# Kernel tuning notes

Hardware: AMD Instinct MI355X
Metric: run time of the kernel (lower is better)

The kernel has to match this reference:

```python
import jax, jax.numpy as jnp
import numpy as np

L, B, S, D, F, H = 4, 2, 1024, 1024, 4096, 16
EPS = 1e-5


def setup_inputs() -> dict:
    key = jax.random.key(0)
    ks = jax.random.split(key, 15)
    w = lambda k, shape, s=0.02: (jax.random.normal(k, shape, jnp.float32) * s)
    inp = {
        "x": jax.random.normal(ks[0], (B, S, D), jnp.float32),
        # stacked per-layer params (scanned over leading L axis)
        "ln1_w": jnp.ones((L, D), jnp.float32),
        "ln1_b": jnp.zeros((L, D), jnp.float32),
        "Wq": w(ks[1], (L, D, D)),
        "Wk": w(ks[2], (L, D, D)),
        "Wv": w(ks[3], (L, D, D)),
        "Wo": w(ks[4], (L, D, D)),
        "bo": jnp.zeros((L, D), jnp.float32),
        "ln2_w": jnp.ones((L, D), jnp.float32),
        "ln2_b": jnp.zeros((L, D), jnp.float32),
        "W1": w(ks[5], (L, D, F)),
        "b1": jnp.zeros((L, F), jnp.float32),
        "W2": w(ks[6], (L, F, D)),
        "b2": jnp.zeros((L, D), jnp.float32),
    }
    return inp


def _layernorm(y, w, b):
    m = jnp.mean(y, axis=-1, keepdims=True)
    v = jnp.mean(jnp.square(y - m), axis=-1, keepdims=True)
    return (y - m) * jax.lax.rsqrt(v + EPS) * w + b


def _block(x, p):
    ln1w, ln1b, wq, wk, wv, wo, bo, ln2w, ln2b, w1, b1, w2, b2 = p
    b, s, d = x.shape
    dh = d // H
    scale = dh ** -0.5
    # --- attention sub-block (pre-norm, residual) ---
    h = _layernorm(x, ln1w, ln1b)
    q = (h @ wq).reshape(b, s, H, dh).transpose(0, 2, 1, 3)  # bhsd
    k = (h @ wk).reshape(b, s, H, dh).transpose(0, 2, 1, 3)
    v = (h @ wv).reshape(b, s, H, dh).transpose(0, 2, 1, 3)
    attn = jax.nn.softmax(jnp.einsum("bhqd,bhkd->bhqk", q, k) * scale, axis=-1)
    o = jnp.einsum("bhqk,bhkd->bhqd", attn, v).transpose(0, 2, 1, 3).reshape(b, s, d)
    x = x + (o @ wo + bo)
    # --- FFN sub-block (pre-norm, residual) ---
    h = _layernorm(x, ln2w, ln2b)
    x = x + (jax.nn.gelu(h @ w1 + b1, approximate=False) @ w2 + b2)
    return x, None


def reference(x, ln1_w, ln1_b, Wq, Wk, Wv, Wo, bo, ln2_w, ln2_b, W1, b1, W2, b2):
    xs = (ln1_w, ln1_b, Wq, Wk, Wv, Wo, bo, ln2_w, ln2_b, W1, b1, W2, b2)
    out, _ = jax.lax.scan(_block, x, xs)
    return out
```

## Files before the change

kernel.cpp:

```cpp
#include <hip/hip_runtime.h>
#include <hip/hip_bf16.h>

using bf16   = __bf16;
using bf16x2 = __attribute__((ext_vector_type(2))) __bf16;
using bf16x4 = __attribute__((ext_vector_type(4))) __bf16;
using bf16x8 = __attribute__((ext_vector_type(8))) __bf16;
using f32x4  = __attribute__((ext_vector_type(4))) float;

constexpr int LAYERS = 4;
constexpr int BATCH  = 2;
constexpr int SEQ    = 1024;
constexpr int DIM    = 1024;
constexpr int FF     = 4096;
constexpr int HEADS  = 16;
constexpr int TOK    = BATCH * SEQ;
constexpr int QKVN   = 3 * DIM;
constexpr float EPS  = 1e-5f;

__device__ __forceinline__ void gload_lds16(const void* g, void* l) {
    __builtin_amdgcn_global_load_lds(
        (const __attribute__((address_space(1))) void*)g,
        (__attribute__((address_space(3))) void*)l, 16, 0, 0);
}

__global__ __launch_bounds__(256) void ln_kernel(
    const float* __restrict__ x, const float* __restrict__ g,
    const float* __restrict__ bt, bf16* __restrict__ out)
{
    __shared__ float red[8];
    const int row = blockIdx.x, t = threadIdx.x;
    const float4 v = ((const float4*)(x + (size_t)row * DIM))[t];

    float s = v.x + v.y + v.z + v.w;
    #pragma unroll
    for (int o = 32; o; o >>= 1) s += __shfl_down(s, o, 64);
    if ((t & 63) == 0) red[t >> 6] = s;
    __syncthreads();
    const float mean = (red[0] + red[1] + red[2] + red[3]) * (1.0f / DIM);

    const float dx = v.x - mean, dy = v.y - mean, dz = v.z - mean, dw = v.w - mean;
    float q = dx * dx + dy * dy + dz * dz + dw * dw;
    #pragma unroll
    for (int o = 32; o; o >>= 1) q += __shfl_down(q, o, 64);
    if ((t & 63) == 0) red[4 + (t >> 6)] = q;
    __syncthreads();
    const float var = (red[4] + red[5] + red[6] + red[7]) * (1.0f / DIM);
    const float rstd = rsqrtf(var + EPS);

    const float4 gg = ((const float4*)g)[t];
    const float4 bb = ((const float4*)bt)[t];
    bf16x4 o4;
    o4[0] = (bf16)(dx * rstd * gg.x + bb.x);
    o4[1] = (bf16)(dy * rstd * gg.y + bb.y);
    o4[2] = (bf16)(dz * rstd * gg.z + bb.z);
    o4[3] = (bf16)(dw * rstd * gg.w + bb.w);
    *(bf16x4*)(out + (size_t)row * DIM + t * 4) = o4;
}

template<bool DO_LN>
__global__ __launch_bounds__(256) void lncomb_kernel(
    float* __restrict__ x, const bf16* __restrict__ p,
    const float* __restrict__ bias, const float* __restrict__ g,
    const float* __restrict__ bt, bf16* __restrict__ out)
{
    __shared__ float red[8];
    const int row = blockIdx.x, t = threadIdx.x;
    float4 v = ((const float4*)(x + (size_t)row * DIM))[t];
    const float4 bv = ((const float4*)bias)[t];
    float a0 = bv.x, a1 = bv.y, a2 = bv.z, a3 = bv.w;
    #pragma unroll
    for (int ks = 0; ks < 4; ++ks) {
        const bf16x4 pp = *(const bf16x4*)(p + (size_t)(ks * TOK + row) * DIM + t * 4);
        a0 += (float)pp[0]; a1 += (float)pp[1];
        a2 += (float)pp[2]; a3 += (float)pp[3];
    }
    v.x += a0; v.y += a1; v.z += a2; v.w += a3;
    ((float4*)(x + (size_t)row * DIM))[t] = v;
    if (!DO_LN) return;

    float s = v.x + v.y + v.z + v.w;
    #pragma unroll
    for (int o = 32; o; o >>= 1) s += __shfl_down(s, o, 64);
    if ((t & 63) == 0) red[t >> 6] = s;
    __syncthreads();
    const float mean = (red[0] + red[1] + red[2] + red[3]) * (1.0f / DIM);

    const float dx = v.x - mean, dy = v.y - mean, dz = v.z - mean, dw = v.w - mean;
    float q = dx * dx + dy * dy + dz * dz + dw * dw;
    #pragma unroll
    for (int o = 32; o; o >>= 1) q += __shfl_down(q, o, 64);
    if ((t & 63) == 0) red[4 + (t >> 6)] = q;
    __syncthreads();
    const float var = (red[4] + red[5] + red[6] + red[7]) * (1.0f / DIM);
    const float rstd = rsqrtf(var + EPS);

    const float4 gg = ((const float4*)g)[t];
    const float4 bb = ((const float4*)bt)[t];
    bf16x4 o4;
    o4[0] = (bf16)(dx * rstd * gg.x + bb.x);
    o4[1] = (bf16)(dy * rstd * gg.y + bb.y);
    o4[2] = (bf16)(dz * rstd * gg.z + bb.z);
    o4[3] = (bf16)(dw * rstd * gg.w + bb.w);
    *(bf16x4*)(out + (size_t)row * DIM + t * 4) = o4;
}

__global__ __launch_bounds__(256) void wtrans_all_kernel(
    const float* __restrict__ Wq, const float* __restrict__ Wk,
    const float* __restrict__ Wv, const float* __restrict__ Wo,
    const float* __restrict__ W1, const float* __restrict__ W2,
    bf16* __restrict__ wqkvt, bf16* __restrict__ wot,
    bf16* __restrict__ w1t, bf16* __restrict__ w2t)
{
    __shared__ float tile[32][33];
    const int bid = blockIdx.x;
    const float* W; bf16* Wt; int N, K, rowoff, bx, by;
    if (bid < 3072) {
        const int seg = bid >> 10, r = bid & 1023;
        W = (seg == 0) ? Wq : (seg == 1) ? Wk : Wv;
        Wt = wqkvt; N = DIM; K = DIM; rowoff = seg * DIM;
        bx = r & 31; by = r >> 5;
    } else if (bid < 4096) {
        const int r = bid - 3072;
        W = Wo; Wt = wot; N = DIM; K = DIM; rowoff = 0;
        bx = r & 31; by = r >> 5;
    } else if (bid < 8192) {
        const int r = bid - 4096;
        W = W1; Wt = w1t; N = FF; K = DIM; rowoff = 0;
        bx = r & 127; by = r >> 7;
    } else {
        const int r = bid - 8192;
        W = W2; Wt = w2t; N = DIM; K = FF; rowoff = 0;
        bx = r & 31; by = r >> 5;
    }
    const int bn = bx * 32, bk = by * 32;
    const int r = threadIdx.x >> 3, c4 = (threadIdx.x & 7) * 4;
    const float4 v = *(const float4*)(W + (size_t)(bk + r) * N + bn + c4);
    tile[r][c4 + 0] = v.x; tile[r][c4 + 1] = v.y;
    tile[r][c4 + 2] = v.z; tile[r][c4 + 3] = v.w;
    __syncthreads();
    bf16x4 o;
    #pragma unroll
    for (int j = 0; j < 4; ++j) o[j] = (bf16)tile[c4 + j][r];
    *(bf16x4*)(Wt + (size_t)(rowoff + bn + r) * K + bk + c4) = o;
}

template<int EPI, int SK>
__global__ __launch_bounds__(256) void gemm_kernel(
    const bf16* __restrict__ A, const bf16* __restrict__ Bt,
    const float* __restrict__ bias, void* __restrict__ outv,
    int M, int N, int Kfull)
{
    constexpr int MR = 2;
    __shared__ bf16 As[2][128 * 32];
    __shared__ bf16 Bs[2][64 * 32];

    const int t    = threadIdx.x;
    const int lane = t & 63;
    const int w    = t >> 6;
    const int wm   = w * 32;
    const int kg   = lane >> 4, lr = lane & 15;
    const int key  = lr & 3;

    const int nwg = gridDim.x;
    const int bid = (blockIdx.x & 7) * (nwg >> 3) + (blockIdx.x >> 3);
    const int nbn = N / 64, nbm = M / 128;
    const int ks  = (SK > 1) ? bid / (nbm * nbn) : 0;
    const int r   = (SK > 1) ? bid % (nbm * nbn) : bid;
    const int bm  = ((SK > 1) ? (r / nbn) : (r % nbm)) * 128;
    const int bn  = ((SK > 1) ? (r % nbn) : (r / nbm)) * 64;

    const int Ksl = Kfull / SK;
    const int kof = ks * Ksl;

    f32x4 acc[MR][4] = {};

    auto stage = [&](int buf, int k0) {
        #pragma unroll
        for (int it = 0; it < 2; ++it) {
            const int ci = it * 256 + t, row = ci >> 2, c = ci & 3;
            gload_lds16(A + (size_t)(bm + row) * Kfull + kof + k0 + ((c ^ (row & 3)) << 3),
                        &As[buf][ci * 8]);
        }
        {
            const int ci = t, row = ci >> 2, c = ci & 3;
            gload_lds16(Bt + (size_t)(bn + row) * Kfull + kof + k0 + ((c ^ (row & 3)) << 3),
                        &Bs[buf][ci * 8]);
        }
    };

    stage(0, 0);
    __syncthreads();

    int cur = 0;
    for (int k0 = 0; k0 < Ksl; k0 += 32) {
        if (k0 + 32 < Ksl) stage(cur ^ 1, k0 + 32);

        bf16x8 af[MR], bfr[4];
        #pragma unroll
        for (int m = 0; m < MR; ++m) {
            const int row = wm + m * 16 + lr;
            af[m] = *(const bf16x8*)(&As[cur][row * 32 + ((kg ^ key) << 3)]);
        }
        #pragma unroll
        for (int n = 0; n < 4; ++n) {
            const int row = n * 16 + lr;
            bfr[n] = *(const bf16x8*)(&Bs[cur][row * 32 + ((kg ^ key) << 3)]);
        }
        #pragma unroll
        for (int m = 0; m < MR; ++m)
            #pragma unroll
            for (int n = 0; n < 4; ++n)
                acc[m][n] = __builtin_amdgcn_mfma_f32_16x16x32_bf16(af[m], bfr[n], acc[m][n], 0, 0, 0);

        __syncthreads();
        cur ^= 1;
    }

    #pragma unroll
    for (int m = 0; m < MR; ++m) {
        const int row = bm + wm + m * 16 + kg * 4;
        #pragma unroll
        for (int n = 0; n < 4; ++n) {
            const int col = bn + n * 16 + lr;
            #pragma unroll
            for (int j = 0; j < 4; ++j) {
                const float vv = acc[m][n][j];
                const size_t idx = (size_t)(row + j) * N + col;
                if (EPI == 0) {
                    ((bf16*)outv)[idx] = (bf16)vv;
                } else if (EPI == 1) {
                    const float z = vv + bias[col];
                    const float gl = 0.5f * z * (1.0f + erff(z * 0.70710678118654752f));
                    ((bf16*)outv)[idx] = (bf16)gl;
                } else {
                    ((bf16*)outv)[(size_t)ks * M * N + idx] = (bf16)vv;
                }
            }
        }
    }
}

__global__ __launch_bounds__(256) void attn_kernel(
    const bf16* __restrict__ qkv, bf16* __restrict__ od)
{
    __shared__ bf16 Ks[2][64][72];
    __shared__ bf16 Vt[2][64][64];
    __shared__ bf16 Ps[4][16][72];

    const int nwg = gridDim.x;
    const int bid = (blockIdx.x & 7) * (nwg >> 3) + (blockIdx.x >> 3);
    const int q0  = (bid & 15) * 64;
    const int bh  = bid >> 4;
    const int b   = bh >> 4, h = bh & 15;
    const int t   = threadIdx.x, w = t >> 6, lane = t & 63;
    const int kg  = lane >> 4, lr = lane & 15;

    const bf16* qbase = qkv + (size_t)b * SEQ * QKVN + h * 64;
    const bf16* kbase = qbase + DIM;
    const bf16* vbase = qbase + 2 * DIM;

    bf16x8 qf0, qf1;
    {
        const bf16* qr = qbase + (size_t)(q0 + w * 16 + lr) * QKVN;
        qf0 = *(const bf16x8*)(qr + kg * 8);
        qf1 = *(const bf16x8*)(qr + 32 + kg * 8);
        #pragma unroll
        for (int j = 0; j < 8; ++j) {
            qf0[j] = (bf16)((float)qf0[j] * 0.125f);
            qf1[j] = (bf16)((float)qf1[j] * 0.125f);
        }
    }

    f32x4 o_acc[4] = {};
    float m_run = -1e30f, l_run = 0.f;

    const int rK = t >> 3, oK = (t & 7) * 8;
    const int rp = t >> 3, cV = t & 7;

    bf16x8 kr0, kr1, vr0, vr1;
    auto loadKV = [&](int kb) {
        kr0 = *(const bf16x8*)(kbase + (size_t)(kb + rK) * QKVN + oK);
        kr1 = *(const bf16x8*)(kbase + (size_t)(kb + 32 + rK) * QKVN + oK);
        vr0 = *(const bf16x8*)(vbase + (size_t)(kb + 2 * rp) * QKVN + cV * 8);
        vr1 = *(const bf16x8*)(vbase + (size_t)(kb + 2 * rp + 1) * QKVN + cV * 8);
    };
    auto storeKV = [&](int buf) {
        *(bf16x8*)&Ks[buf][rK][oK]      = kr0;
        *(bf16x8*)&Ks[buf][32 + rK][oK] = kr1;
        #pragma unroll
        for (int j = 0; j < 8; ++j) {
            bf16x2 p; p[0] = vr0[j]; p[1] = vr1[j];
            const int d  = cV * 8 + j;
            const int dw = (((rp >> 2) ^ (j ^ cV)) << 2) | (rp & 3);
            *(bf16x2*)((char*)&Vt[buf][d][0] + dw * 4) = p;
        }
    };

    loadKV(0);
    storeKV(0);
    __syncthreads();

    int cur = 0;
    for (int kb = 0; kb < SEQ; kb += 64) {
        const bool more = (kb + 64 < SEQ);
        if (more) loadKV(kb + 64);

        f32x4 s[4] = {};
        __builtin_amdgcn_s_setprio(1);
        #pragma unroll
        for (int n = 0; n < 4; ++n) {
            const bf16x8 kf0 = *(const bf16x8*)&Ks[cur][n * 16 + lr][kg * 8];
            const bf16x8 kf1 = *(const bf16x8*)&Ks[cur][n * 16 + lr][32 + kg * 8];
            s[n] = __builtin_amdgcn_mfma_f32_16x16x32_bf16(kf0, qf0, s[n], 0, 0, 0);
            s[n] = __builtin_amdgcn_mfma_f32_16x16x32_bf16(kf1, qf1, s[n], 0, 0, 0);
        }
        __builtin_amdgcn_s_setprio(0);

        float pmax = -1e30f;
        #pragma unroll
        for (int n = 0; n < 4; ++n)
            #pragma unroll
            for (int j = 0; j < 4; ++j) pmax = fmaxf(pmax, s[n][j]);
        pmax = fmaxf(pmax, __shfl_xor(pmax, 16, 64));
        pmax = fmaxf(pmax, __shfl_xor(pmax, 32, 64));

        if (!__all(pmax <= m_run + 8.0f)) {
            const float mn   = fmaxf(m_run, pmax);
            const float corr = __expf(m_run - mn);
            m_run = mn;
            l_run *= corr;
            #pragma unroll
            for (int nd = 0; nd < 4; ++nd)
                #pragma unroll
                for (int j = 0; j < 4; ++j) o_acc[nd][j] *= corr;
        }

        float rs = 0.f;
        #pragma unroll
        for (int n = 0; n < 4; ++n)
            #pragma unroll
            for (int j = 0; j < 4; ++j) {
                const float e = __expf(s[n][j] - m_run);
                s[n][j] = e; rs += e;
            }
        rs += __shfl_xor(rs, 16, 64);
        rs += __shfl_xor(rs, 32, 64);
        l_run += rs;

        #pragma unroll
        for (int n = 0; n < 4; ++n) {
            bf16x4 pw;
            #pragma unroll
            for (int j = 0; j < 4; ++j) pw[j] = (bf16)s[n][j];
            *(bf16x4*)&Ps[w][lr][n * 16 + kg * 4] = pw;
        }

        const bf16x8 pf0 = *(const bf16x8*)&Ps[w][lr][kg * 8];
        const bf16x8 pf1 = *(const bf16x8*)&Ps[w][lr][32 + kg * 8];
        __builtin_amdgcn_s_setprio(1);
        #pragma unroll
        for (int nd = 0; nd < 4; ++nd) {
            const int d   = nd * 16 + lr;
            const int keyv = (d ^ (d >> 3)) & 7;
            const bf16x8 vf0 = *(const bf16x8*)((const char*)&Vt[cur][d][0] + ((kg ^ keyv) << 4));
            const bf16x8 vf1 = *(const bf16x8*)((const char*)&Vt[cur][d][0] + (((4 + kg) ^ keyv) << 4));
            o_acc[nd] = __builtin_amdgcn_mfma_f32_16x16x32_bf16(vf0, pf0, o_acc[nd], 0, 0, 0);
            o_acc[nd] = __builtin_amdgcn_mfma_f32_16x16x32_bf16(vf1, pf1, o_acc[nd], 0, 0, 0);
        }
        __builtin_amdgcn_s_setprio(0);

        if (more) storeKV(cur ^ 1);
        __syncthreads();
        cur ^= 1;
    }

    const float inv = 1.0f / l_run;
    bf16* ob = od + (size_t)(b * SEQ + q0 + w * 16 + lr) * DIM + h * 64;
    #pragma unroll
    for (int nd = 0; nd < 4; ++nd) {
        bf16x4 o4;
        #pragma unroll
        for (int j = 0; j < 4; ++j) o4[j] = (bf16)(o_acc[nd][j] * inv);
        *(bf16x4*)(ob + nd * 16 + kg * 4) = o4;
    }
}

extern "C" void kernel_launch(void* const* d_in, const int* in_sizes, int n_in,
                              void* d_out, int out_size, void* d_ws, size_t ws_size,
                              hipStream_t stream)
{
    const float* x    = (const float*)d_in[0];
    const float* ln1w = (const float*)d_in[1];
    const float* ln1b = (const float*)d_in[2];
    const float* Wq   = (const float*)d_in[3];
    const float* Wk   = (const float*)d_in[4];
    const float* Wv   = (const float*)d_in[5];
    const float* Wo   = (const float*)d_in[6];
    const float* bo   = (const float*)d_in[7];
    const float* ln2w = (const float*)d_in[8];
    const float* ln2b = (const float*)d_in[9];
    const float* W1   = (const float*)d_in[10];
    const float* b1   = (const float*)d_in[11];
    const float* W2   = (const float*)d_in[12];
    const float* b2   = (const float*)d_in[13];

    char* ws = (char*)d_ws;
    float* xbuf  = (float*)(ws);
    bf16*  hbuf  = (bf16*)(ws + (8ull  << 20));
    bf16*  qkvb  = (bf16*)(ws + (12ull << 20));
    bf16*  obuf  = (bf16*)(ws + (24ull << 20));
    bf16*  gbuf  = (bf16*)(ws + (28ull << 20));
    bf16*  wqkvt = (bf16*)(ws + (44ull << 20));
    bf16*  wot   = (bf16*)(ws + (50ull << 20));
    bf16*  w1t   = (bf16*)(ws + (52ull << 20));
    bf16*  w2t   = (bf16*)(ws + (60ull << 20));
    bf16*  pbuf  = (bf16*)(ws + (68ull << 20));

    hipMemcpyAsync(xbuf, x, (size_t)TOK * DIM * sizeof(float),
                   hipMemcpyDeviceToDevice, stream);

    const size_t DD = (size_t)DIM * DIM, DF = (size_t)DIM * FF;
    for (int l = 0; l < LAYERS; ++l) {
        wtrans_all_kernel<<<12288, 256, 0, stream>>>(
            Wq + l * DD, Wk + l * DD, Wv + l * DD, Wo + l * DD,
            W1 + l * DF, W2 + l * DF, wqkvt, wot, w1t, w2t);

        if (l == 0)
            ln_kernel<<<TOK, 256, 0, stream>>>(xbuf, ln1w, ln1b, hbuf);

        gemm_kernel<0, 1><<<16 * 48, 256, 0, stream>>>(
            hbuf, wqkvt, nullptr, qkvb, TOK, QKVN, DIM);

        attn_kernel<<<512, 256, 0, stream>>>(qkvb, obuf);

        gemm_kernel<3, 4><<<16 * 16 * 4, 256, 0, stream>>>(
            obuf, wot, nullptr, pbuf, TOK, DIM, DIM);

        lncomb_kernel<true><<<TOK, 256, 0, stream>>>(
            xbuf, pbuf, bo + l * DIM, ln2w + l * DIM, ln2b + l * DIM, hbuf);

        gemm_kernel<1, 1><<<16 * 64, 256, 0, stream>>>(
            hbuf, w1t, b1 + l * FF, gbuf, TOK, FF, DIM);

        gemm_kernel<3, 4><<<16 * 16 * 4, 256, 0, stream>>>(
            gbuf, w2t, nullptr, pbuf, TOK, DIM, FF);

        if (l + 1 < LAYERS)
            lncomb_kernel<true><<<TOK, 256, 0, stream>>>(
                xbuf, pbuf, b2 + l * DIM, ln1w + (l + 1) * DIM, ln1b + (l + 1) * DIM, hbuf);
        else
            lncomb_kernel<false><<<TOK, 256, 0, stream>>>(
                xbuf, pbuf, b2 + l * DIM, nullptr, nullptr, nullptr);
    }

    hipMemcpyAsync(d_out, xbuf, (size_t)TOK * DIM * sizeof(float),
                   hipMemcpyDeviceToDevice, stream);
}
```

Baseline: 598.2 us.

## Widen weight-transpose tiles, fix GEMM LDS swizzle, async-stage K in attention

The weight-transpose kernel now uses 64x64 tiles with 16-byte bf16x8 stores, cutting the launch from 12288 to 3072 blocks. The GEMM LDS XOR swizzle key changes from row&3 to (row>>1)&3 to reduce bank conflicts on fragment reads. The attention kernel loads K tiles directly into a swizzled LDS buffer with global_load_lds instead of going through registers, while V keeps the register path. Together these aim to cut transpose overhead and LDS conflicts, at the risk of a swizzle mismatch between the loads and the fragment reads.

```diff
diff --git a/kernel.cpp b/kernel.cpp
--- a/kernel.cpp
+++ b/kernel.cpp
@@ -111,37 +111,50 @@
     bf16* __restrict__ wqkvt, bf16* __restrict__ wot,
     bf16* __restrict__ w1t, bf16* __restrict__ w2t)
 {
-    __shared__ float tile[32][33];
+    __shared__ float tile[64][65];
     const int bid = blockIdx.x;
     const float* W; bf16* Wt; int N, K, rowoff, bx, by;
-    if (bid < 3072) {
-        const int seg = bid >> 10, r = bid & 1023;
+    if (bid < 768) {
+        const int seg = bid >> 8, r = bid & 255;
         W = (seg == 0) ? Wq : (seg == 1) ? Wk : Wv;
         Wt = wqkvt; N = DIM; K = DIM; rowoff = seg * DIM;
-        bx = r & 31; by = r >> 5;
-    } else if (bid < 4096) {
-        const int r = bid - 3072;
+        bx = r & 15; by = r >> 4;
+    } else if (bid < 1024) {
+        const int r = bid - 768;
         W = Wo; Wt = wot; N = DIM; K = DIM; rowoff = 0;
-        bx = r & 31; by = r >> 5;
-    } else if (bid < 8192) {
-        const int r = bid - 4096;
+        bx = r & 15; by = r >> 4;
+    } else if (bid < 2048) {
+        const int r = bid - 1024;
         W = W1; Wt = w1t; N = FF; K = DIM; rowoff = 0;
-        bx = r & 127; by = r >> 7;
+        bx = r & 63; by = r >> 6;
     } else {
-        const int r = bid - 8192;
+        const int r = bid - 2048;
         W = W2; Wt = w2t; N = DIM; K = FF; rowoff = 0;
-        bx = r & 31; by = r >> 5;
-    }
-    const int bn = bx * 32, bk = by * 32;
-    const int r = threadIdx.x >> 3, c4 = (threadIdx.x & 7) * 4;
-    const float4 v = *(const float4*)(W + (size_t)(bk + r) * N + bn + c4);
-    tile[r][c4 + 0] = v.x; tile[r][c4 + 1] = v.y;
-    tile[r][c4 + 2] = v.z; tile[r][c4 + 3] = v.w;
-    __syncthreads();
-    bf16x4 o;
-    #pragma unroll
-    for (int j = 0; j < 4; ++j) o[j] = (bf16)tile[c4 + j][r];
-    *(bf16x4*)(Wt + (size_t)(rowoff + bn + r) * K + bk + c4) = o;
+        bx = r & 15; by = r >> 4;
+    }
+    const int bn = bx * 64, bk = by * 64;
+    {
+        const int r16 = threadIdx.x >> 4, c4 = (threadIdx.x & 15) * 4;
+        #pragma unroll
+        for (int i = 0; i < 4; ++i) {
+            const int kr = r16 + i * 16;
+            const float4 v = *(const float4*)(W + (size_t)(bk + kr) * N + bn + c4);
+            tile[kr][c4 + 0] = v.x; tile[kr][c4 + 1] = v.y;
+            tile[kr][c4 + 2] = v.z; tile[kr][c4 + 3] = v.w;
+        }
+    }
+    __syncthreads();
+    {
+        const int n = threadIdx.x >> 2, ch = threadIdx.x & 3;
+        #pragma unroll
+        for (int i = 0; i < 2; ++i) {
+            const int k0 = (ch + i * 4) * 8;
+            bf16x8 o;
+            #pragma unroll
+            for (int j = 0; j < 8; ++j) o[j] = (bf16)tile[k0 + j][n];
+            *(bf16x8*)(Wt + (size_t)(rowoff + bn + n) * K + bk + k0) = o;
+        }
+    }
 }
 
 template<int EPI, int SK>
@@ -159,7 +172,7 @@
     const int w    = t >> 6;
     const int wm   = w * 32;
     const int kg   = lane >> 4, lr = lane & 15;
-    const int key  = lr & 3;
+    const int key  = (lr >> 1) & 3;
 
     const int nwg = gridDim.x;
     const int bid = (blockIdx.x & 7) * (nwg >> 3) + (blockIdx.x >> 3);
@@ -178,12 +191,12 @@
         #pragma unroll
         for (int it = 0; it < 2; ++it) {
             const int ci = it * 256 + t, row = ci >> 2, c = ci & 3;
-            gload_lds16(A + (size_t)(bm + row) * Kfull + kof + k0 + ((c ^ (row & 3)) << 3),
+            gload_lds16(A + (size_t)(bm + row) * Kfull + kof + k0 + ((c ^ ((row >> 1) & 3)) << 3),
                         &As[buf][ci * 8]);
         }
         {
             const int ci = t, row = ci >> 2, c = ci & 3;
-            gload_lds16(Bt + (size_t)(bn + row) * Kfull + kof + k0 + ((c ^ (row & 3)) << 3),
+            gload_lds16(Bt + (size_t)(bn + row) * Kfull + kof + k0 + ((c ^ ((row >> 1) & 3)) << 3),
                         &Bs[buf][ci * 8]);
         }
     };
@@ -243,7 +256,7 @@
 __global__ __launch_bounds__(256) void attn_kernel(
     const bf16* __restrict__ qkv, bf16* __restrict__ od)
 {
-    __shared__ bf16 Ks[2][64][72];
+    __shared__ bf16 Ks[2][64 * 64];
     __shared__ bf16 Vt[2][64][64];
     __shared__ bf16 Ps[4][16][72];
 
@@ -274,19 +287,22 @@
     f32x4 o_acc[4] = {};
     float m_run = -1e30f, l_run = 0.f;
 
-    const int rK = t >> 3, oK = (t & 7) * 8;
     const int rp = t >> 3, cV = t & 7;
 
-    bf16x8 kr0, kr1, vr0, vr1;
-    auto loadKV = [&](int kb) {
-        kr0 = *(const bf16x8*)(kbase + (size_t)(kb + rK) * QKVN + oK);
-        kr1 = *(const bf16x8*)(kbase + (size_t)(kb + 32 + rK) * QKVN + oK);
+    bf16x8 vr0, vr1;
+    auto loadV = [&](int kb) {
         vr0 = *(const bf16x8*)(vbase + (size_t)(kb + 2 * rp) * QKVN + cV * 8);
         vr1 = *(const bf16x8*)(vbase + (size_t)(kb + 2 * rp + 1) * QKVN + cV * 8);
     };
-    auto storeKV = [&](int buf) {
-        *(bf16x8*)&Ks[buf][rK][oK]      = kr0;
-        *(bf16x8*)&Ks[buf][32 + rK][oK] = kr1;
+    auto stageK = [&](int buf, int kb) {
+        #pragma unroll
+        for (int i = 0; i < 2; ++i) {
+            const int ci = i * 256 + t, row = ci >> 3, c = ci & 7;
+            gload_lds16(kbase + (size_t)(kb + row) * QKVN + ((c ^ (row & 7)) << 3),
+                        &Ks[buf][ci * 8]);
+        }
+    };
+    auto storeV = [&](int buf) {
         #pragma unroll
         for (int j = 0; j < 8; ++j) {
             bf16x2 p; p[0] = vr0[j]; p[1] = vr1[j];
@@ -296,21 +312,23 @@
         }
     };
 
-    loadKV(0);
-    storeKV(0);
+    loadV(0);
+    stageK(0, 0);
+    storeV(0);
     __syncthreads();
 
     int cur = 0;
     for (int kb = 0; kb < SEQ; kb += 64) {
         const bool more = (kb + 64 < SEQ);
-        if (more) loadKV(kb + 64);
+        if (more) { loadV(kb + 64); stageK(cur ^ 1, kb + 64); }
 
         f32x4 s[4] = {};
         __builtin_amdgcn_s_setprio(1);
         #pragma unroll
         for (int n = 0; n < 4; ++n) {
-            const bf16x8 kf0 = *(const bf16x8*)&Ks[cur][n * 16 + lr][kg * 8];
-            const bf16x8 kf1 = *(const bf16x8*)&Ks[cur][n * 16 + lr][32 + kg * 8];
+            const int row = n * 16 + lr;
+            const bf16x8 kf0 = *(const bf16x8*)&Ks[cur][row * 64 + ((kg ^ (lr & 7)) << 3)];
+            const bf16x8 kf1 = *(const bf16x8*)&Ks[cur][row * 64 + (((4 + kg) ^ (lr & 7)) << 3)];
             s[n] = __builtin_amdgcn_mfma_f32_16x16x32_bf16(kf0, qf0, s[n], 0, 0, 0);
             s[n] = __builtin_amdgcn_mfma_f32_16x16x32_bf16(kf1, qf1, s[n], 0, 0, 0);
         }
@@ -369,7 +387,7 @@
         }
         __builtin_amdgcn_s_setprio(0);
 
-        if (more) storeKV(cur ^ 1);
+        if (more) storeV(cur ^ 1);
         __syncthreads();
         cur ^= 1;
     }
@@ -421,7 +439,7 @@
 
     const size_t DD = (size_t)DIM * DIM, DF = (size_t)DIM * FF;
     for (int l = 0; l < LAYERS; ++l) {
-        wtrans_all_kernel<<<12288, 256, 0, stream>>>(
+        wtrans_all_kernel<<<3072, 256, 0, stream>>>(
             Wq + l * DD, Wk + l * DD, Wv + l * DD, Wo + l * DD,
             W1 + l * DF, W2 + l * DF, wqkvt, wot, w1t, w2t);
 
```

Result: no change. 606.8 us (+1.4%).
